# Kernel optimization log

Hardware: AMD Instinct MI355X
Metric: run time of the kernel (lower is better)

Reference implementation:

```python
import jax, jax.numpy as jnp
import numpy as np

N = 100000
E = 1200000
D = 64  # g_dim == h2_dim, heads=1


def setup_inputs() -> dict:
    key = jax.random.key(0)
    ks = jax.random.split(key, 12)
    s = 1.0 / np.sqrt(D)
    node_features = jax.random.normal(ks[0], (N, D), dtype=jnp.float32)
    edge_index = jax.random.randint(ks[1], (2, E), 0, N, dtype=jnp.int64)
    edge_type = jax.random.randint(ks[2], (E,), 0, 4, dtype=jnp.int64)
    Wq = jax.random.uniform(ks[3], (D, D), jnp.float32, -s, s)
    bq = jax.random.uniform(ks[4], (D,), jnp.float32, -s, s)
    Wk = jax.random.uniform(ks[5], (D, D), jnp.float32, -s, s)
    bk = jax.random.uniform(ks[6], (D,), jnp.float32, -s, s)
    Wv = jax.random.uniform(ks[7], (D, D), jnp.float32, -s, s)
    bv = jax.random.uniform(ks[8], (D,), jnp.float32, -s, s)
    Wskip = jax.random.uniform(ks[9], (D, D), jnp.float32, -s, s)
    bskip = jax.random.uniform(ks[10], (D,), jnp.float32, -s, s)
    return dict(node_features=node_features, edge_index=edge_index,
                edge_type=edge_type, Wq=Wq, bq=bq, Wk=Wk, bk=bk,
                Wv=Wv, bv=bv, Wskip=Wskip, bskip=bskip)


def _transformer_conv(x, edge_index, Wq, bq, Wk, bk, Wv, bv, Wskip, bskip):
    src, dst = edge_index[0], edge_index[1]
    q = x @ Wq + bq          # [N, D] queries (for targets)
    k = x @ Wk + bk          # [N, D] keys (for sources)
    v = x @ Wv + bv          # [N, D] values (for sources)
    scale = 1.0 / jnp.sqrt(jnp.asarray(D, x.dtype))
    # per-edge attention logits: (q_dst . k_src) / sqrt(D)   [E]
    logits = jnp.sum(q[dst] * k[src], axis=-1) * scale
    # segment softmax over incoming edges of each destination node
    seg_max = jax.ops.segment_max(logits, dst, num_segments=N)
    seg_max = jnp.where(jnp.isfinite(seg_max), seg_max, 0.0)
    ex = jnp.exp(logits - seg_max[dst])
    seg_sum = jax.ops.segment_sum(ex, dst, num_segments=N)
    alpha = ex / (seg_sum[dst] + 1e-16)                      # [E]
    # attention-weighted scatter-aggregate of source values
    out = jax.ops.segment_sum(alpha[:, None] * v[src], dst, num_segments=N)
    # root/skip connection
    return out + x @ Wskip + bskip


def reference(node_features, edge_index, edge_type, Wq, bq, Wk, bk, Wv, bv, Wskip, bskip):
    # edge_type is accepted but unused, matching the original forward.
    return _transformer_conv(node_features, edge_index, Wq, bq, Wk, bk, Wv, bv, Wskip, bskip)
```

## Files before the change

kernel.cpp:

```cpp
#include <hip/hip_runtime.h>
#include <hip/hip_fp16.h>

#define D 64
#define BSH 9
#define SPLIT_CH 4096
#define NH 512

typedef _Float16 f16x2 __attribute__((ext_vector_type(2)));

__device__ __forceinline__ float fdot2f(f16x2 a, f16x2 b, float c) {
#if __has_builtin(__builtin_amdgcn_fdot2)
    return __builtin_amdgcn_fdot2(a, b, c, false);
#else
    return fmaf((float)a.x, (float)b.x, fmaf((float)a.y, (float)b.y, c));
#endif
}

__device__ __forceinline__ f16x2 shxor_h2(f16x2 v, int m) {
    int i = __builtin_bit_cast(int, v);
    i = __shfl_xor(i, m);
    return __builtin_bit_cast(f16x2, i);
}

__global__ __launch_bounds__(256) void k_prep(
    const float* __restrict__ Wq, const float* __restrict__ Wk,
    const float* __restrict__ Wv, const float* __restrict__ Wsk,
    __half2* __restrict__ whd, int* __restrict__ ghist)
{
    const int idx = blockIdx.x * 256 + threadIdx.x;
    if (blockIdx.x < 32) {
        const int g  = idx >> 11;
        const int r  = idx & 2047;
        const int d2 = r >> 6;
        const int c  = r & 63;
        const float* W = (g == 0) ? Wq : (g == 1) ? Wk : (g == 2) ? Wv : Wsk;
        whd[idx] = __floats2half2_rn(W[(2 * d2) * 64 + c],
                                     W[(2 * d2 + 1) * 64 + c]);
    } else {
        ghist[threadIdx.x] = 0;
    }
}

__global__ __launch_bounds__(256) void k_histlin(
    const float* __restrict__ x, const __half2* __restrict__ whd,
    const float* __restrict__ bq, const float* __restrict__ bk,
    const float* __restrict__ bv, const float* __restrict__ bsk,
    const int* __restrict__ ei, int* __restrict__ ghist,
    __half2* __restrict__ qh, __half2* __restrict__ kvh,
    float* __restrict__ out, int n, int e_cnt, int NL)
{
    __shared__ f16x2 xsh[32][33];
    const int t = threadIdx.x;

    if (blockIdx.x >= NL) {
        int* h = (int*)xsh;
        h[t] = 0;
        __syncthreads();
        const int hb    = blockIdx.x - NL;
        const int chunk = (e_cnt + NH - 1) / NH;
        const int c0    = hb * chunk;
        const int c1    = min(c0 + chunk, e_cnt);
        for (int i = c0 + t; i < c1; i += 256)
            atomicAdd(&h[ei[e_cnt + i] >> BSH], 1);
        __syncthreads();
        if (h[t]) atomicAdd(&ghist[t], h[t]);
        return;
    }

    const int row0 = blockIdx.x * 32;
    {
        const float4* xg = (const float4*)(x + (size_t)row0 * 64);
        if (row0 + 32 <= n) {
#pragma unroll
            for (int i0 = 0; i0 < 2; ++i0) {
                const int i = t + i0 * 256;
                const float4 v = xg[i];
                const int row = i >> 4, dq = (i & 15) << 1;
                xsh[row][dq]     = f16x2{(_Float16)v.x, (_Float16)v.y};
                xsh[row][dq + 1] = f16x2{(_Float16)v.z, (_Float16)v.w};
            }
        } else {
            for (int i = t; i < 512; i += 256) {
                const int row = i >> 4;
                if (row0 + row < n) {
                    const float4 v = xg[i];
                    const int dq = (i & 15) << 1;
                    xsh[row][dq]     = f16x2{(_Float16)v.x, (_Float16)v.y};
                    xsh[row][dq + 1] = f16x2{(_Float16)v.z, (_Float16)v.w};
                }
            }
        }
    }
    __syncthreads();

    const int wr = t >> 6;
    const int c  = t & 63;
    const f16x2* wq2 = (const f16x2*)whd;
    const f16x2* wk2 = (const f16x2*)(whd + 2048);
    const f16x2* wv2 = (const f16x2*)(whd + 4096);
    const f16x2* ws2 = (const f16x2*)(whd + 6144);

    float aq[8], ak[8], av[8], ask[8];
#pragma unroll
    for (int j = 0; j < 8; ++j) {
        aq[j] = bq[c]; ak[j] = bk[c]; av[j] = bv[c]; ask[j] = bsk[c];
    }

#pragma unroll 4
    for (int d2 = 0; d2 < 32; ++d2) {
        const f16x2 wqp = wq2[d2 * 64 + c];
        const f16x2 wkp = wk2[d2 * 64 + c];
        const f16x2 wvp = wv2[d2 * 64 + c];
        const f16x2 wsp = ws2[d2 * 64 + c];
#pragma unroll
        for (int j = 0; j < 8; ++j) {
            const f16x2 xp = xsh[wr * 8 + j][d2];
            aq[j]  = fdot2f(xp, wqp, aq[j]);
            ak[j]  = fdot2f(xp, wkp, ak[j]);
            av[j]  = fdot2f(xp, wvp, av[j]);
            ask[j] = fdot2f(xp, wsp, ask[j]);
        }
    }

#pragma unroll
    for (int j = 0; j < 8; ++j) {
        const int row = row0 + wr * 8 + j;
        if (row < n) {
            const float aqs = aq[j] * 0.18033688f;
            const float aqx = __shfl_xor(aqs, 1);
            const float akx = __shfl_xor(ak[j], 1);
            const float avx = __shfl_xor(av[j], 1);
            out[(size_t)row * 64 + c] = ask[j];
            if ((c & 1) == 0) {
                qh [(size_t)row * 32 + (c >> 1)]      = __floats2half2_rn(aqs, aqx);
                kvh[(size_t)row * 64 + (c >> 1)]      = __floats2half2_rn(ak[j], akx);
            } else {
                kvh[(size_t)row * 64 + 32 + (c >> 1)] = __floats2half2_rn(avx, av[j]);
            }
        }
    }
}

__global__ __launch_bounds__(256) void k_scanb(
    const int* __restrict__ ghist, int* __restrict__ gbase,
    int* __restrict__ gcur)
{
    __shared__ int s[256];
    const int t = threadIdx.x;
    const int v = ghist[t];
    s[t] = v;
    __syncthreads();
    for (int off = 1; off < 256; off <<= 1) {
        const int add = (t >= off) ? s[t - off] : 0;
        __syncthreads();
        s[t] += add;
        __syncthreads();
    }
    const int ex = s[t] - v;
    gbase[t] = ex;
    gcur[t]  = ex;
}

__global__ __launch_bounds__(256) void k_split(
    const int* __restrict__ ei, int* __restrict__ gcur,
    unsigned* __restrict__ epack, int e_cnt)
{
    __shared__ unsigned vals[SPLIT_CH];
    __shared__ int addr[SPLIT_CH];
    __shared__ int hist[256], start[256], cur[256], base[256], s2[256];

    const int t  = threadIdx.x;
    const int e0 = blockIdx.x * SPLIT_CH;
    const int cnt = min(SPLIT_CH, e_cnt - e0);

    hist[t] = 0;
    __syncthreads();
    for (int i = t; i < cnt; i += 256)
        atomicAdd(&hist[ei[e_cnt + e0 + i] >> BSH], 1);
    __syncthreads();

    {
        const int v = hist[t];
        s2[t] = v;
        __syncthreads();
        for (int off = 1; off < 256; off <<= 1) {
            const int add = (t >= off) ? s2[t - off] : 0;
            __syncthreads();
            s2[t] += add;
            __syncthreads();
        }
        start[t] = s2[t] - v;
        cur[t]   = s2[t] - v;
        base[t]  = v ? atomicAdd(&gcur[t], v) : 0;
    }
    __syncthreads();

    for (int i = t; i < cnt; i += 256) {
        const int s = ei[e0 + i];
        const int d = ei[e_cnt + e0 + i];
        const int b = d >> BSH;
        const int r = atomicAdd(&cur[b], 1);
        vals[r] = ((unsigned)s << BSH) | (unsigned)(d & 511);
        addr[r] = base[b] + (r - start[b]);
    }
    __syncthreads();

    for (int i = t; i < cnt; i += 256)
        epack[addr[i]] = vals[i];
}

__global__ __launch_bounds__(512) void k_nodesort(
    const unsigned* __restrict__ epack, const int* __restrict__ gbase,
    const int* __restrict__ ghist, int* __restrict__ esrc,
    int* __restrict__ endoff, int n)
{
    __shared__ int h[512], cur[512], s[512];
    const int b    = blockIdx.x;
    const int t    = threadIdx.x;
    const int base = gbase[b];
    const int cnt  = ghist[b];

    h[t] = 0;
    __syncthreads();
    for (int i = t; i < cnt; i += 512)
        atomicAdd(&h[epack[base + i] & 511], 1);
    __syncthreads();

    const int v = h[t];
    s[t] = v;
    __syncthreads();
    for (int off = 1; off < 512; off <<= 1) {
        const int add = (t >= off) ? s[t - off] : 0;
        __syncthreads();
        s[t] += add;
        __syncthreads();
    }
    cur[t] = s[t] - v;
    const int node = (b << BSH) + t;
    if (node < n) endoff[node] = base + s[t];
    __syncthreads();

    for (int i = t; i < cnt; i += 512) {
        const unsigned p = epack[base + i];
        const int r = atomicAdd(&cur[p & 511], 1);
        esrc[base + r] = (int)(p >> BSH);
    }
}

__global__ __launch_bounds__(256) void k_attn(
    const uint4* __restrict__ qh4, const uint4* __restrict__ kv4,
    const int* __restrict__ endoff, const int* __restrict__ esrc,
    float* __restrict__ out, int n)
{
    const int t = threadIdx.x;
    const int node = blockIdx.x * 4 + (t >> 6);
    if (node >= n) return;
    const int lane = t & 63;
    const int g = lane >> 3;
    const int l = lane & 7;

    const int beg = (node == 0) ? 0 : endoff[node - 1];
    const int end = endoff[node];

    float4 o0 = make_float4(0.f, 0.f, 0.f, 0.f);
    float4 o1 = o0;
    if (g == 0) {
        o0 = ((const float4*)out)[(size_t)node * 16 + 2 * l];
        o1 = ((const float4*)out)[(size_t)node * 16 + 2 * l + 1];
    }

    const uint4 qu = qh4[(size_t)node * 8 + l];
    const f16x2* qp = (const f16x2*)&qu;

    f16x2 a0 = {(_Float16)0.f, (_Float16)0.f};
    f16x2 a1 = a0, a2 = a0, a3 = a0;
    float den = 0.f;

    for (int b2 = beg; b2 < end; b2 += 8) {
        const int i = b2 + g;
        const int s = esrc[min(i, end - 1)];
        const uint4 ku = kv4[(size_t)s * 16 + l];
        const uint4 vu = kv4[(size_t)s * 16 + 8 + l];
        const f16x2* kp = (const f16x2*)&ku;
        const f16x2* vp = (const f16x2*)&vu;

        float d = fdot2f(qp[0], kp[0], 0.f);
        d = fdot2f(qp[1], kp[1], d);
        d = fdot2f(qp[2], kp[2], d);
        d = fdot2f(qp[3], kp[3], d);
        d += __shfl_xor(d, 1);
        d += __shfl_xor(d, 2);
        d += __shfl_xor(d, 4);

        const float e = (i < end) ? exp2f(d) : 0.f;
        den += e;
        const _Float16 eh = (_Float16)e;
        const f16x2 e2 = {eh, eh};
        a0 += e2 * vp[0];
        a1 += e2 * vp[1];
        a2 += e2 * vp[2];
        a3 += e2 * vp[3];
    }

#pragma unroll
    for (int m = 8; m <= 32; m <<= 1) {
        den += __shfl_xor(den, m);
        a0 += shxor_h2(a0, m);
        a1 += shxor_h2(a1, m);
        a2 += shxor_h2(a2, m);
        a3 += shxor_h2(a3, m);
    }

    if (g == 0) {
        const float inv = 1.f / (den + 1e-16f);
        float4 r0, r1;
        r0.x = o0.x + (float)a0.x * inv;
        r0.y = o0.y + (float)a0.y * inv;
        r0.z = o0.z + (float)a1.x * inv;
        r0.w = o0.w + (float)a1.y * inv;
        r1.x = o1.x + (float)a2.x * inv;
        r1.y = o1.y + (float)a2.y * inv;
        r1.z = o1.z + (float)a3.x * inv;
        r1.w = o1.w + (float)a3.y * inv;
        ((float4*)out)[(size_t)node * 16 + 2 * l]     = r0;
        ((float4*)out)[(size_t)node * 16 + 2 * l + 1] = r1;
    }
}

extern "C" void kernel_launch(void* const* d_in, const int* in_sizes, int n_in,
                              void* d_out, int out_size, void* d_ws, size_t ws_size,
                              hipStream_t stream)
{
    const float* x   = (const float*)d_in[0];
    const int*   ei  = (const int*)d_in[1];
    const float* Wq  = (const float*)d_in[3];
    const float* bq  = (const float*)d_in[4];
    const float* Wk  = (const float*)d_in[5];
    const float* bk  = (const float*)d_in[6];
    const float* Wv  = (const float*)d_in[7];
    const float* bv  = (const float*)d_in[8];
    const float* Wsk = (const float*)d_in[9];
    const float* bsk = (const float*)d_in[10];
    float* out = (float*)d_out;

    const int n     = in_sizes[0] / D;
    const int e_cnt = in_sizes[1] / 2;
    const int nbkt  = (n + 511) >> BSH;
    const int NL    = (n + 31) / 32;

    __half2*  qh     = (__half2*)d_ws;
    __half2*  kvh    = qh + (size_t)n * 32;
    int*      esrc   = (int*)(kvh + (size_t)n * 64);
    unsigned* epack  = (unsigned*)(esrc + e_cnt);
    int*      endoff = (int*)(epack + e_cnt);
    int*      ghist  = endoff + n;
    int*      gbase  = ghist + 256;
    int*      gcur   = gbase + 256;
    __half2*  whd    = (__half2*)(gcur + 256);

    k_prep<<<33, 256, 0, stream>>>(Wq, Wk, Wv, Wsk, whd, ghist);

    k_histlin<<<NL + NH, 256, 0, stream>>>(
        x, whd, bq, bk, bv, bsk, ei, ghist, qh, kvh, out, n, e_cnt, NL);

    k_scanb<<<1, 256, 0, stream>>>(ghist, gbase, gcur);

    k_split<<<(e_cnt + SPLIT_CH - 1) / SPLIT_CH, 256, 0, stream>>>(
        ei, gcur, epack, e_cnt);

    k_nodesort<<<nbkt, 512, 0, stream>>>(
        epack, gbase, ghist, esrc, endoff, n);

    k_attn<<<(n + 3) / 4, 256, 0, stream>>>(
        (const uint4*)qh, (const uint4*)kvh, endoff, esrc, out, n);
}
```

Measured before the change: 137.6 us.

## Use MFMA for node projections and fold bucket scan into split/sort kernels

Replaces the fdot2-based fused Q/K/V/skip projection with 16x16x32 f16 MFMA instructions, using weights prepacked into fragment layout with the query scale and biases folded in during prep. Removes the single-block k_scanb launch by having k_split and k_nodesort each recompute the bucket prefix sum locally, with a zeroed per-bucket cursor. This cuts one kernel launch and the scalar dot-product cost of the linear stage. In exchange every split and sort block does redundant scans, and the linear stage now uses smaller 16-node tiles.

```diff
diff --git a/kernel.cpp b/kernel.cpp
--- a/kernel.cpp
+++ b/kernel.cpp
@@ -5,8 +5,11 @@
 #define BSH 9
 #define SPLIT_CH 4096
 #define NH 512
+#define QSCALE 0.18033688f
 
 typedef _Float16 f16x2 __attribute__((ext_vector_type(2)));
+typedef _Float16 f16x8 __attribute__((ext_vector_type(8)));
+typedef float f32x4 __attribute__((ext_vector_type(4)));
 
 __device__ __forceinline__ float fdot2f(f16x2 a, f16x2 b, float c) {
 #if __has_builtin(__builtin_amdgcn_fdot2)
@@ -22,41 +25,61 @@
     return __builtin_bit_cast(f16x2, i);
 }
 
+__device__ __forceinline__ unsigned packh2(float a, float b) {
+    __half2 h = __floats2half2_rn(a, b);
+    return __builtin_bit_cast(unsigned, h);
+}
+
 __global__ __launch_bounds__(256) void k_prep(
     const float* __restrict__ Wq, const float* __restrict__ Wk,
     const float* __restrict__ Wv, const float* __restrict__ Wsk,
-    __half2* __restrict__ whd, int* __restrict__ ghist)
-{
-    const int idx = blockIdx.x * 256 + threadIdx.x;
-    if (blockIdx.x < 32) {
-        const int g  = idx >> 11;
-        const int r  = idx & 2047;
-        const int d2 = r >> 6;
-        const int c  = r & 63;
-        const float* W = (g == 0) ? Wq : (g == 1) ? Wk : (g == 2) ? Wv : Wsk;
-        whd[idx] = __floats2half2_rn(W[(2 * d2) * 64 + c],
-                                     W[(2 * d2 + 1) * 64 + c]);
-    } else {
-        ghist[threadIdx.x] = 0;
-    }
-}
-
-__global__ __launch_bounds__(256) void k_histlin(
-    const float* __restrict__ x, const __half2* __restrict__ whd,
     const float* __restrict__ bq, const float* __restrict__ bk,
     const float* __restrict__ bv, const float* __restrict__ bsk,
+    unsigned* __restrict__ wpk, float* __restrict__ ball,
+    int* __restrict__ ghist, int* __restrict__ gcur0)
+{
+    const int t = threadIdx.x;
+    if (blockIdx.x < 32) {
+        const int u    = blockIdx.x * 256 + t;
+        const int i2   = u & 3;
+        const int lane = (u >> 2) & 63;
+        const int ks   = (u >> 8) & 1;
+        const int mt   = u >> 9;
+        const int ncol = mt * 16 + (lane & 15);
+        const int k0   = ks * 32 + ((lane >> 4) << 3) + (i2 << 1);
+        const float* W; int c; float sc = 1.f;
+        if      (ncol <  64) { W = Wq;  c = ncol;       sc = QSCALE; }
+        else if (ncol < 128) { W = Wk;  c = ncol - 64;  }
+        else if (ncol < 192) { W = Wv;  c = ncol - 128; }
+        else                 { W = Wsk; c = ncol - 192; }
+        wpk[u] = packh2(W[k0 * 64 + c] * sc, W[(k0 + 1) * 64 + c] * sc);
+    } else {
+        ghist[t] = 0;
+        gcur0[t] = 0;
+        float b;
+        if      (t <  64) b = bq[t] * QSCALE;
+        else if (t < 128) b = bk[t - 64];
+        else if (t < 192) b = bv[t - 128];
+        else              b = bsk[t - 192];
+        ball[t] = b;
+    }
+}
+
+__global__ __launch_bounds__(256) void k_histlin(
+    const float* __restrict__ x, const unsigned* __restrict__ wpk,
+    const float* __restrict__ ball,
     const int* __restrict__ ei, int* __restrict__ ghist,
-    __half2* __restrict__ qh, __half2* __restrict__ kvh,
-    float* __restrict__ out, int n, int e_cnt, int NL)
-{
-    __shared__ f16x2 xsh[32][33];
+    unsigned* __restrict__ qh, unsigned* __restrict__ kvh,
+    float* __restrict__ out, int n, int e_cnt, int NLIN)
+{
+    __shared__ __align__(16) _Float16 xsh[16][72];
     const int t = threadIdx.x;
 
-    if (blockIdx.x >= NL) {
+    if (blockIdx.x >= NLIN) {
         int* h = (int*)xsh;
         h[t] = 0;
         __syncthreads();
-        const int hb    = blockIdx.x - NL;
+        const int hb    = blockIdx.x - NLIN;
         const int chunk = (e_cnt + NH - 1) / NH;
         const int c0    = hb * chunk;
         const int c1    = min(c0 + chunk, e_cnt);
@@ -67,107 +90,78 @@
         return;
     }
 
-    const int row0 = blockIdx.x * 32;
+    const int node0 = blockIdx.x * 16;
     {
-        const float4* xg = (const float4*)(x + (size_t)row0 * 64);
-        if (row0 + 32 <= n) {
+        const float4* xg = (const float4*)(x + (size_t)node0 * 64);
+        const int row = t >> 4, c4 = (t & 15) << 2;
+        if (node0 + row < n) {
+            const float4 v = xg[t];
+            f16x2* dst = (f16x2*)&xsh[row][c4];
+            dst[0] = f16x2{(_Float16)v.x, (_Float16)v.y};
+            dst[1] = f16x2{(_Float16)v.z, (_Float16)v.w};
+        }
+    }
+    __syncthreads();
+
+    const int w  = t >> 6;
+    const int l  = t & 63;
+    const int nd = l & 15;
+    const int kg = l >> 4;
+
+    f32x4 acc0 = {0.f, 0.f, 0.f, 0.f};
+    f32x4 acc1 = acc0, acc2 = acc0, acc3 = acc0;
+    const uint4* wpk4 = (const uint4*)wpk;
+
 #pragma unroll
-            for (int i0 = 0; i0 < 2; ++i0) {
-                const int i = t + i0 * 256;
-                const float4 v = xg[i];
-                const int row = i >> 4, dq = (i & 15) << 1;
-                xsh[row][dq]     = f16x2{(_Float16)v.x, (_Float16)v.y};
-                xsh[row][dq + 1] = f16x2{(_Float16)v.z, (_Float16)v.w};
-            }
+    for (int ks = 0; ks < 2; ++ks) {
+        const f16x8 bfrag = *(const f16x8*)&xsh[nd][ks * 32 + kg * 8];
+        const int fb = (w * 4 * 2 + ks) * 64 + l;
+        const f16x8 a0 = __builtin_bit_cast(f16x8, wpk4[fb]);
+        const f16x8 a1 = __builtin_bit_cast(f16x8, wpk4[fb + 128]);
+        const f16x8 a2 = __builtin_bit_cast(f16x8, wpk4[fb + 256]);
+        const f16x8 a3 = __builtin_bit_cast(f16x8, wpk4[fb + 384]);
+        acc0 = __builtin_amdgcn_mfma_f32_16x16x32_f16(a0, bfrag, acc0, 0, 0, 0);
+        acc1 = __builtin_amdgcn_mfma_f32_16x16x32_f16(a1, bfrag, acc1, 0, 0, 0);
+        acc2 = __builtin_amdgcn_mfma_f32_16x16x32_f16(a2, bfrag, acc2, 0, 0, 0);
+        acc3 = __builtin_amdgcn_mfma_f32_16x16x32_f16(a3, bfrag, acc3, 0, 0, 0);
+    }
+
+    const int node = node0 + nd;
+    if (node >= n) return;
+
+    f32x4 accs[4] = {acc0, acc1, acc2, acc3};
+#pragma unroll
+    for (int m4 = 0; m4 < 4; ++m4) {
+        const int gc = (w * 4 + m4) * 16 + kg * 4;
+        const float4 bb = ((const float4*)ball)[gc >> 2];
+        const float v0 = accs[m4][0] + bb.x;
+        const float v1 = accs[m4][1] + bb.y;
+        const float v2 = accs[m4][2] + bb.z;
+        const float v3 = accs[m4][3] + bb.w;
+        if (w == 3) {
+            ((float4*)out)[(size_t)node * 16 + ((gc - 192) >> 2)] =
+                make_float4(v0, v1, v2, v3);
         } else {
-            for (int i = t; i < 512; i += 256) {
-                const int row = i >> 4;
-                if (row0 + row < n) {
-                    const float4 v = xg[i];
-                    const int dq = (i & 15) << 1;
-                    xsh[row][dq]     = f16x2{(_Float16)v.x, (_Float16)v.y};
-                    xsh[row][dq + 1] = f16x2{(_Float16)v.z, (_Float16)v.w};
-                }
-            }
+            uint2 u;
+            u.x = packh2(v0, v1);
+            u.y = packh2(v2, v3);
+            if (w == 0)
+                ((uint2*)qh)[(size_t)node * 16 + (gc >> 2)] = u;
+            else if (w == 1)
+                ((uint2*)kvh)[(size_t)node * 32 + ((gc - 64) >> 2)] = u;
+            else
+                ((uint2*)kvh)[(size_t)node * 32 + 16 + ((gc - 128) >> 2)] = u;
         }
     }
-    __syncthreads();
-
-    const int wr = t >> 6;
-    const int c  = t & 63;
-    const f16x2* wq2 = (const f16x2*)whd;
-    const f16x2* wk2 = (const f16x2*)(whd + 2048);
-    const f16x2* wv2 = (const f16x2*)(whd + 4096);
-    const f16x2* ws2 = (const f16x2*)(whd + 6144);
-
-    float aq[8], ak[8], av[8], ask[8];
-#pragma unroll
-    for (int j = 0; j < 8; ++j) {
-        aq[j] = bq[c]; ak[j] = bk[c]; av[j] = bv[c]; ask[j] = bsk[c];
-    }
-
-#pragma unroll 4
-    for (int d2 = 0; d2 < 32; ++d2) {
-        const f16x2 wqp = wq2[d2 * 64 + c];
-        const f16x2 wkp = wk2[d2 * 64 + c];
-        const f16x2 wvp = wv2[d2 * 64 + c];
-        const f16x2 wsp = ws2[d2 * 64 + c];
-#pragma unroll
-        for (int j = 0; j < 8; ++j) {
-            const f16x2 xp = xsh[wr * 8 + j][d2];
-            aq[j]  = fdot2f(xp, wqp, aq[j]);
-            ak[j]  = fdot2f(xp, wkp, ak[j]);
-            av[j]  = fdot2f(xp, wvp, av[j]);
-            ask[j] = fdot2f(xp, wsp, ask[j]);
-        }
-    }
-
-#pragma unroll
-    for (int j = 0; j < 8; ++j) {
-        const int row = row0 + wr * 8 + j;
-        if (row < n) {
-            const float aqs = aq[j] * 0.18033688f;
-            const float aqx = __shfl_xor(aqs, 1);
-            const float akx = __shfl_xor(ak[j], 1);
-            const float avx = __shfl_xor(av[j], 1);
-            out[(size_t)row * 64 + c] = ask[j];
-            if ((c & 1) == 0) {
-                qh [(size_t)row * 32 + (c >> 1)]      = __floats2half2_rn(aqs, aqx);
-                kvh[(size_t)row * 64 + (c >> 1)]      = __floats2half2_rn(ak[j], akx);
-            } else {
-                kvh[(size_t)row * 64 + 32 + (c >> 1)] = __floats2half2_rn(avx, av[j]);
-            }
-        }
-    }
-}
-
-__global__ __launch_bounds__(256) void k_scanb(
-    const int* __restrict__ ghist, int* __restrict__ gbase,
-    int* __restrict__ gcur)
-{
-    __shared__ int s[256];
-    const int t = threadIdx.x;
-    const int v = ghist[t];
-    s[t] = v;
-    __syncthreads();
-    for (int off = 1; off < 256; off <<= 1) {
-        const int add = (t >= off) ? s[t - off] : 0;
-        __syncthreads();
-        s[t] += add;
-        __syncthreads();
-    }
-    const int ex = s[t] - v;
-    gbase[t] = ex;
-    gcur[t]  = ex;
 }
 
 __global__ __launch_bounds__(256) void k_split(
-    const int* __restrict__ ei, int* __restrict__ gcur,
-    unsigned* __restrict__ epack, int e_cnt)
+    const int* __restrict__ ei, const int* __restrict__ ghist,
+    int* __restrict__ gcur0, unsigned* __restrict__ epack, int e_cnt)
 {
     __shared__ unsigned vals[SPLIT_CH];
     __shared__ int addr[SPLIT_CH];
-    __shared__ int hist[256], start[256], cur[256], base[256], s2[256];
+    __shared__ int hist[256], start[256], cur[256], base[256], s2[256], sg[256];
 
     const int t  = threadIdx.x;
     const int e0 = blockIdx.x * SPLIT_CH;
@@ -181,17 +175,21 @@
 
     {
         const int v = hist[t];
+        const int g = ghist[t];
         s2[t] = v;
+        sg[t] = g;
         __syncthreads();
         for (int off = 1; off < 256; off <<= 1) {
-            const int add = (t >= off) ? s2[t - off] : 0;
+            const int a1 = (t >= off) ? s2[t - off] : 0;
+            const int a2 = (t >= off) ? sg[t - off] : 0;
             __syncthreads();
-            s2[t] += add;
+            s2[t] += a1;
+            sg[t] += a2;
             __syncthreads();
         }
         start[t] = s2[t] - v;
         cur[t]   = s2[t] - v;
-        base[t]  = v ? atomicAdd(&gcur[t], v) : 0;
+        base[t]  = v ? (sg[t] - g + atomicAdd(&gcur0[t], v)) : 0;
     }
     __syncthreads();
 
@@ -210,14 +208,25 @@
 }
 
 __global__ __launch_bounds__(512) void k_nodesort(
-    const unsigned* __restrict__ epack, const int* __restrict__ gbase,
-    const int* __restrict__ ghist, int* __restrict__ esrc,
-    int* __restrict__ endoff, int n)
+    const unsigned* __restrict__ epack, const int* __restrict__ ghist,
+    int* __restrict__ esrc, int* __restrict__ endoff, int n)
 {
     __shared__ int h[512], cur[512], s[512];
-    const int b    = blockIdx.x;
-    const int t    = threadIdx.x;
-    const int base = gbase[b];
+    __shared__ int sbase;
+    const int b = blockIdx.x;
+    const int t = threadIdx.x;
+
+    s[t] = (t < 256) ? ghist[t] : 0;
+    __syncthreads();
+    for (int off = 1; off < 512; off <<= 1) {
+        const int add = (t >= off) ? s[t - off] : 0;
+        __syncthreads();
+        s[t] += add;
+        __syncthreads();
+    }
+    if (t == 0) sbase = (b == 0) ? 0 : s[b - 1];
+    __syncthreads();
+    const int base = sbase;
     const int cnt  = ghist[b];
 
     h[t] = 0;
@@ -346,30 +355,29 @@
     const int n     = in_sizes[0] / D;
     const int e_cnt = in_sizes[1] / 2;
     const int nbkt  = (n + 511) >> BSH;
-    const int NL    = (n + 31) / 32;
-
-    __half2*  qh     = (__half2*)d_ws;
-    __half2*  kvh    = qh + (size_t)n * 32;
+    const int NLIN  = (n + 15) / 16;
+
+    unsigned* qh     = (unsigned*)d_ws;
+    unsigned* kvh    = qh + (size_t)n * 32;
     int*      esrc   = (int*)(kvh + (size_t)n * 64);
     unsigned* epack  = (unsigned*)(esrc + e_cnt);
     int*      endoff = (int*)(epack + e_cnt);
     int*      ghist  = endoff + n;
-    int*      gbase  = ghist + 256;
-    int*      gcur   = gbase + 256;
-    __half2*  whd    = (__half2*)(gcur + 256);
-
-    k_prep<<<33, 256, 0, stream>>>(Wq, Wk, Wv, Wsk, whd, ghist);
-
-    k_histlin<<<NL + NH, 256, 0, stream>>>(
-        x, whd, bq, bk, bv, bsk, ei, ghist, qh, kvh, out, n, e_cnt, NL);
-
-    k_scanb<<<1, 256, 0, stream>>>(ghist, gbase, gcur);
+    int*      gcur0  = ghist + 256;
+    float*    ball   = (float*)(gcur0 + 256);
+    unsigned* wpk    = (unsigned*)(ball + 256);
+
+    k_prep<<<33, 256, 0, stream>>>(
+        Wq, Wk, Wv, Wsk, bq, bk, bv, bsk, wpk, ball, ghist, gcur0);
+
+    k_histlin<<<NLIN + NH, 256, 0, stream>>>(
+        x, wpk, ball, ei, ghist, qh, kvh, out, n, e_cnt, NLIN);
 
     k_split<<<(e_cnt + SPLIT_CH - 1) / SPLIT_CH, 256, 0, stream>>>(
-        ei, gcur, epack, e_cnt);
+        ei, ghist, gcur0, epack, e_cnt);
 
     k_nodesort<<<nbkt, 512, 0, stream>>>(
-        epack, gbase, ghist, esrc, endoff, n);
+        epack, ghist, esrc, endoff, n);
 
     k_attn<<<(n + 3) / 4, 256, 0, stream>>>(
         (const uint4*)qh, (const uint4*)kvh, endoff, esrc, out, n);
```

After: 126.9 us. -7.8%, faster.
